# Kernel tuning notes

Measured on AMD Instinct MI355X. Metric: run time of the kernel, lower is better.

The kernel has to match this reference:

```python
import jax, jax.numpy as jnp
import numpy as np

PS = 4          # patch_size (square)
STRIDE = 2
PAD = (PS - 1) // 2
HEADS = 8
DIM = 256       # attn_dim == dim (kv_dim > dim, dim_reduc=1)
KV_DIM = 512
HD = DIM // HEADS
SCALE = HD ** -0.5
NP2 = PS * PS   # 16 elements per window


def _unfold(x, k, s, p):
    """torch.nn.functional.unfold: (B,C,H,W) -> (B, C*k*k, Ho*Wo)."""
    B, C, H, W = x.shape
    xp = jnp.pad(x, ((0, 0), (0, 0), (p, p), (p, p)))
    Ho = (H + 2 * p - k) // s + 1
    Wo = (W + 2 * p - k) // s + 1
    r = (jnp.arange(Ho) * s)[:, None] + jnp.arange(k)   # (Ho,k)
    c = (jnp.arange(Wo) * s)[:, None] + jnp.arange(k)   # (Wo,k)
    pt = xp[:, :, r][:, :, :, :, c]                     # (B,C,Ho,k,Wo,k)
    pt = pt.transpose(0, 1, 3, 5, 2, 4)                 # (B,C,k,k,Ho,Wo)
    return pt.reshape(B, C * k * k, Ho * Wo)


def _fold(y, C, Hout, Wout, k, s, p):
    """torch.nn.functional.fold: (B, C*k*k, Ho*Wo) -> (B,C,Hout,Wout), overlap-add."""
    B = y.shape[0]
    Ho = (Hout + 2 * p - k) // s + 1
    Wo = (Wout + 2 * p - k) // s + 1
    pt = y.reshape(B, C, k, k, Ho, Wo).transpose(0, 1, 4, 2, 5, 3)  # (B,C,Ho,k,Wo,k)
    r = (jnp.arange(Ho) * s)[:, None] + jnp.arange(k)
    c = (jnp.arange(Wo) * s)[:, None] + jnp.arange(k)
    out = jnp.zeros((B, C, Hout + 2 * p, Wout + 2 * p), y.dtype)
    out = out.at[:, :, r[:, :, None, None], c[None, None, :, :]].add(pt)
    return out[:, :, p:Hout + p, p:Wout + p]


def _patch_softmax(attn, Ht, Wt, Hb, Wb):
    """Normalize exp(attn) by per-bottom-pixel sums computed via a fold/unfold round trip
    (faithful to the original, including its reshape layout)."""
    a = jnp.exp(attn)                                                # (B*HtWt, H, 16, 1)
    s = a.reshape(-1, Ht * Wt, HEADS, NP2).transpose(0, 2, 3, 1)     # (B, H, 16, HtWt)
    s = s.reshape(-1, NP2, Ht * Wt)                                  # (B*H, 16, HtWt)
    s = _fold(s, 1, Hb, Wb, PS, STRIDE, PAD)                         # (B*H, 1, Hb, Wb)
    s = _unfold(s, PS, STRIDE, PAD).transpose(0, 2, 1)               # (B*H, HtWt, 16)
    s = jnp.where(s == 0, jnp.ones((), s.dtype), s)
    return a / s.reshape(-1, HEADS, NP2, 1)


def _forward(Xt, Xb, q_w, kv_w, proj_w, proj_b, rel_init, rel_bias, Ht, Wt, Hb, Wb):
    B, _, C = Xb.shape
    # im2col: gather 4x4 windows of the fine map, one window per coarse token
    Xbp = Xb.transpose(0, 2, 1).reshape(B, C, Hb, Wb)
    Xbp = _unfold(Xbp, PS, STRIDE, PAD)                              # (B, C*16, Ht*Wt)
    Xbp = Xbp.reshape(B, C, NP2, Ht * Wt).transpose(0, 3, 2, 1)
    Xbp = Xbp.reshape(B * Ht * Wt, NP2, C)                           # queries (top_down)
    Xtq = Xt.reshape(-1, 1, Xt.shape[-1])                            # (B*HtWt, 1, kv_dim)

    q = (Xbp @ q_w.T).reshape(-1, NP2, HEADS, HD).transpose(0, 2, 1, 3)  # (BHW,H,16,hd)
    kv = (Xtq @ kv_w.T).reshape(-1, 1, 2, HEADS, HD).transpose(2, 0, 3, 1, 4)
    k, v = kv[0], kv[1]                                              # (BHW,H,1,hd)

    attn = (q @ jnp.swapaxes(k, -2, -1)) * SCALE                     # (BHW,H,16,1)
    attn = attn + rel_init[:, None] + rel_bias[:, None]
    attn = _patch_softmax(attn, Ht, Wt, Hb, Wb)

    out = (attn @ v).transpose(0, 2, 1, 3).reshape(-1, NP2, DIM)     # (BHW,16,DIM)
    out = out.reshape(B, Ht * Wt, NP2, DIM).transpose(0, 3, 2, 1)
    out = out.reshape(B, DIM * NP2, Ht * Wt)
    out = _fold(out, DIM, Hb, Wb, PS, STRIDE, PAD)                   # (B,DIM,Hb,Wb)
    out = out.transpose(0, 2, 3, 1).reshape(B, Hb * Wb, DIM)
    return out @ proj_w.T + proj_b


def setup_inputs() -> dict:
    key = jax.random.key(0)
    ks = jax.random.split(key, 7)
    B, Ht, Wt, Hb, Wb = 4, 64, 64, 128, 128
    return {
        "Xt": jax.random.normal(ks[0], (B, Ht * Wt, KV_DIM), jnp.float32),
        "Xb": jax.random.normal(ks[1], (B, Hb * Wb, DIM), jnp.float32),
        "q_w": jax.random.normal(ks[2], (DIM, DIM), jnp.float32) * 0.02,
        "kv_w": jax.random.normal(ks[3], (2 * DIM, KV_DIM), jnp.float32) * 0.02,
        "proj_w": jax.random.normal(ks[4], (DIM, DIM), jnp.float32) * 0.02,
        "proj_b": jnp.zeros((DIM,), jnp.float32),
        "rel_init": jax.random.normal(ks[5], (NP2,), jnp.float32) * 0.02,
        "rel_bias": jax.random.normal(ks[6], (NP2,), jnp.float32) * 0.02,
        "Ht": Ht, "Wt": Wt, "Hb": Hb, "Wb": Wb,
    }


def reference(Xt, Xb, q_w, kv_w, proj_w, proj_b, rel_init, rel_bias, Ht, Wt, Hb, Wb):
    return _forward(Xt, Xb, q_w, kv_w, proj_w, proj_b, rel_init, rel_bias, Ht, Wt, Hb, Wb)
```

## Files before the change

kernel.cpp:

```cpp
#include <hip/hip_runtime.h>
#include <math.h>

constexpr int B_    = 4;
constexpr int HT    = 64,  WT = 64;
constexpr int HB    = 128, WB = 128;
constexpr int DIM   = 256;
constexpr int KVD   = 512;
constexpr int HEADS = 8;
constexpr int NP2   = 16;
constexpr int NPIX  = HB * WB;
constexpr int NWIN  = HT * WT;
constexpr float SCALE = 0.17677669529663687f;

using bf16x8 = __attribute__((ext_vector_type(8))) short;
using f32x4  = __attribute__((ext_vector_type(4))) float;

__device__ __forceinline__ unsigned short f2bf(float f) {
  union { float f; unsigned u; } v; v.f = f;
  unsigned r = v.u + 0x7fffu + ((v.u >> 16) & 1u);
  return (unsigned short)(r >> 16);
}

constexpr int NXT4  = B_ * NWIN * KVD / 4;
constexpr int NQW4  = DIM * DIM / 4;
constexpr int NKVW4 = KVD * KVD / 4;
constexpr int NCAST4 = NXT4 + NQW4 + NKVW4 + NQW4;

__global__ __launch_bounds__(256) void cast_all(
    const float* __restrict__ Xt, const float* __restrict__ qw,
    const float* __restrict__ kvw, const float* __restrict__ pw,
    unsigned short* __restrict__ Xth, unsigned short* __restrict__ qwh,
    unsigned short* __restrict__ kvwh, unsigned short* __restrict__ pwh)
{
  const int i = blockIdx.x * 256 + threadIdx.x;
  const float* src; unsigned short* dst; int off;
  if (i < NXT4)                     { src = Xt;  dst = Xth;  off = i; }
  else if (i < NXT4 + NQW4)         { src = qw;  dst = qwh;  off = i - NXT4; }
  else if (i < NXT4 + NQW4 + NKVW4) { src = kvw; dst = kvwh; off = i - NXT4 - NQW4; }
  else                              { src = pw;  dst = pwh;  off = i - NXT4 - NQW4 - NKVW4; }
  float4 v = ((const float4*)src)[off];
  ushort4 o;
  o.x = f2bf(v.x); o.y = f2bf(v.y); o.z = f2bf(v.z); o.w = f2bf(v.w);
  ((ushort4*)dst)[off] = o;
}

__global__ __launch_bounds__(256) void gemm_af32(
    const float* __restrict__ A, const unsigned short* __restrict__ Bw,
    unsigned short* __restrict__ C, int M, int N, int K)
{
  __shared__ unsigned short Ash[128 * 32];
  __shared__ unsigned short Bsh[128 * 32];

  const int tid  = threadIdx.x;
  const int wave = tid >> 6;
  const int lane = tid & 63;
  const int m0 = blockIdx.x * 128;
  const int n0 = blockIdx.y * 128;
  const int wm = (wave >> 1) * 64;
  const int wn = (wave & 1) * 64;

  const int c0 = wave * 64 + lane;
  const int c1 = 256 + c0;
  const int r0 = c0 >> 2, k0off = (c0 & 3) * 8;
  const int r1 = c1 >> 2, k1off = (c1 & 3) * 8;
  const int ldsOff0 = wave * 1024;
  const int ldsOff1 = 4096 + wave * 1024;

  f32x4 acc[4][4];
#pragma unroll
  for (int i = 0; i < 4; ++i)
#pragma unroll
    for (int j = 0; j < 4; ++j) { f32x4 z = {0.f, 0.f, 0.f, 0.f}; acc[i][j] = z; }

  const int fr = lane & 15;
  const int fk = (lane >> 4) * 8;

  for (int kk = 0; kk < K; kk += 32) {
    __syncthreads();
#pragma unroll
    for (int u = 0; u < 4; ++u) {
      const int c   = tid + u * 256;
      const int row = c >> 3;
      const int kq  = (c & 7) * 4;
      float4 v = *(const float4*)(A + (size_t)(m0 + row) * K + kk + kq);
      uint2 pk;
      pk.x = (unsigned)f2bf(v.x) | ((unsigned)f2bf(v.y) << 16);
      pk.y = (unsigned)f2bf(v.z) | ((unsigned)f2bf(v.w) << 16);
      *(uint2*)&Ash[row * 32 + kq] = pk;
    }
    const unsigned short* b0 = Bw + (size_t)(n0 + r0) * K + kk + k0off;
    const unsigned short* b1 = Bw + (size_t)(n0 + r1) * K + kk + k1off;
    __builtin_amdgcn_global_load_lds(
        (const __attribute__((address_space(1))) unsigned int*)b0,
        (__attribute__((address_space(3))) unsigned int*)((char*)Bsh + ldsOff0),
        16, 0, 0);
    __builtin_amdgcn_global_load_lds(
        (const __attribute__((address_space(1))) unsigned int*)b1,
        (__attribute__((address_space(3))) unsigned int*)((char*)Bsh + ldsOff1),
        16, 0, 0);
    __syncthreads();

    bf16x8 af[4], bfr[4];
#pragma unroll
    for (int t = 0; t < 4; ++t) {
      af[t]  = *(const bf16x8*)&Ash[(wm + t * 16 + fr) * 32 + fk];
      bfr[t] = *(const bf16x8*)&Bsh[(wn + t * 16 + fr) * 32 + fk];
    }
#pragma unroll
    for (int mt = 0; mt < 4; ++mt)
#pragma unroll
      for (int nt = 0; nt < 4; ++nt)
        acc[mt][nt] = __builtin_amdgcn_mfma_f32_16x16x32_bf16(
            af[mt], bfr[nt], acc[mt][nt], 0, 0, 0);
  }

  const int col0 = lane & 15;
  const int rb   = (lane >> 4) * 4;
#pragma unroll
  for (int mt = 0; mt < 4; ++mt)
#pragma unroll
    for (int nt = 0; nt < 4; ++nt) {
      const int col = n0 + wn + nt * 16 + col0;
#pragma unroll
      for (int r = 0; r < 4; ++r) {
        const int row = m0 + wm + mt * 16 + rb + r;
        C[(size_t)row * N + col] = f2bf(acc[mt][nt][r]);
      }
    }
}

template<bool BF16_OUT, bool BIAS>
__global__ __launch_bounds__(256) void gemm_bf16(
    const unsigned short* __restrict__ A, const unsigned short* __restrict__ Bw,
    const float* __restrict__ bias, void* __restrict__ C,
    int M, int N, int K)
{
  __shared__ unsigned short Ash[128 * 32];
  __shared__ unsigned short Bsh[128 * 32];

  const int tid  = threadIdx.x;
  const int wave = tid >> 6;
  const int lane = tid & 63;
  const int m0 = blockIdx.x * 128;
  const int n0 = blockIdx.y * 128;
  const int wm = (wave >> 1) * 64;
  const int wn = (wave & 1) * 64;

  const int c0 = wave * 64 + lane;
  const int c1 = 256 + c0;
  const int r0 = c0 >> 2, k0off = (c0 & 3) * 8;
  const int r1 = c1 >> 2, k1off = (c1 & 3) * 8;
  const int ldsOff0 = wave * 1024;
  const int ldsOff1 = 4096 + wave * 1024;

  f32x4 acc[4][4];
#pragma unroll
  for (int i = 0; i < 4; ++i)
#pragma unroll
    for (int j = 0; j < 4; ++j) { f32x4 z = {0.f, 0.f, 0.f, 0.f}; acc[i][j] = z; }

  const int fr = lane & 15;
  const int fk = (lane >> 4) * 8;

  for (int kk = 0; kk < K; kk += 32) {
    __syncthreads();
    const unsigned short* a0 = A  + (size_t)(m0 + r0) * K + kk + k0off;
    const unsigned short* a1 = A  + (size_t)(m0 + r1) * K + kk + k1off;
    const unsigned short* b0 = Bw + (size_t)(n0 + r0) * K + kk + k0off;
    const unsigned short* b1 = Bw + (size_t)(n0 + r1) * K + kk + k1off;
    __builtin_amdgcn_global_load_lds(
        (const __attribute__((address_space(1))) unsigned int*)a0,
        (__attribute__((address_space(3))) unsigned int*)((char*)Ash + ldsOff0),
        16, 0, 0);
    __builtin_amdgcn_global_load_lds(
        (const __attribute__((address_space(1))) unsigned int*)a1,
        (__attribute__((address_space(3))) unsigned int*)((char*)Ash + ldsOff1),
        16, 0, 0);
    __builtin_amdgcn_global_load_lds(
        (const __attribute__((address_space(1))) unsigned int*)b0,
        (__attribute__((address_space(3))) unsigned int*)((char*)Bsh + ldsOff0),
        16, 0, 0);
    __builtin_amdgcn_global_load_lds(
        (const __attribute__((address_space(1))) unsigned int*)b1,
        (__attribute__((address_space(3))) unsigned int*)((char*)Bsh + ldsOff1),
        16, 0, 0);
    __syncthreads();

    bf16x8 af[4], bfr[4];
#pragma unroll
    for (int t = 0; t < 4; ++t) {
      af[t]  = *(const bf16x8*)&Ash[(wm + t * 16 + fr) * 32 + fk];
      bfr[t] = *(const bf16x8*)&Bsh[(wn + t * 16 + fr) * 32 + fk];
    }
#pragma unroll
    for (int mt = 0; mt < 4; ++mt)
#pragma unroll
      for (int nt = 0; nt < 4; ++nt)
        acc[mt][nt] = __builtin_amdgcn_mfma_f32_16x16x32_bf16(
            af[mt], bfr[nt], acc[mt][nt], 0, 0, 0);
  }

  const int col0 = lane & 15;
  const int rb   = (lane >> 4) * 4;
#pragma unroll
  for (int mt = 0; mt < 4; ++mt)
#pragma unroll
    for (int nt = 0; nt < 4; ++nt) {
      const int col = n0 + wn + nt * 16 + col0;
      float bv = BIAS ? bias[col] : 0.f;
#pragma unroll
      for (int r = 0; r < 4; ++r) {
        const int row = m0 + wm + mt * 16 + rb + r;
        const float v = acc[mt][nt][r] + bv;
        if (BF16_OUT) ((unsigned short*)C)[(size_t)row * N + col] = f2bf(v);
        else          ((float*)C)[(size_t)row * N + col] = v;
      }
    }
}

__global__ __launch_bounds__(256) void es_kernel(
    const unsigned short* __restrict__ Qh, const unsigned short* __restrict__ KVh,
    const float* __restrict__ rel_init, const float* __restrict__ rel_bias,
    float* __restrict__ E, float* __restrict__ S)
{
  const int idx = blockIdx.x * 256 + threadIdx.x;
  const int h = idx & 7;
  const int x = (idx >> 3) & 127;
  const int y = (idx >> 10) & 127;
  const int b = idx >> 17;

  const uint4* qp = (const uint4*)(Qh + ((size_t)((b << 14) + y * WB + x)) * DIM + h * 32);
  uint4 q0 = qp[0], q1 = qp[1], q2 = qp[2], q3 = qp[3];
  const unsigned qa[16] = {q0.x,q0.y,q0.z,q0.w, q1.x,q1.y,q1.z,q1.w,
                           q2.x,q2.y,q2.z,q2.w, q3.x,q3.y,q3.z,q3.w};

  const int ilo = max(0, (y - 1) >> 1), ihi = min(HT - 1, (y + 1) >> 1);
  const int jlo = max(0, (x - 1) >> 1), jhi = min(WT - 1, (x + 1) >> 1);

  float s = 0.f;
  for (int i = ilo; i <= ihi; ++i)
    for (int j = jlo; j <= jhi; ++j) {
      const int w = i * WT + j;
      const int p = (y + 1 - 2 * i) * 4 + (x + 1 - 2 * j);
      const uint4* kp = (const uint4*)(KVh + ((size_t)((b << 12) + w)) * KVD + h * 32);
      uint4 k0 = kp[0], k1 = kp[1], k2 = kp[2], k3 = kp[3];
      const unsigned ka[16] = {k0.x,k0.y,k0.z,k0.w, k1.x,k1.y,k1.z,k1.w,
                               k2.x,k2.y,k2.z,k2.w, k3.x,k3.y,k3.z,k3.w};
      float acc = 0.f;
#pragma unroll
      for (int q = 0; q < 16; ++q) {
        acc = fmaf(__uint_as_float(qa[q] << 16),
                   __uint_as_float(ka[q] << 16), acc);
        acc = fmaf(__uint_as_float(qa[q] & 0xffff0000u),
                   __uint_as_float(ka[q] & 0xffff0000u), acc);
      }
      const float e = expf(acc * SCALE + rel_init[p] + rel_bias[p]);
      E[((size_t)((b << 12) + w)) * 128 + h * NP2 + p] = e;
      s += e;
    }
  S[(size_t)((b * HEADS + h) << 14) + y * WB + x] = s;
}

__global__ __launch_bounds__(256) void r_kernel(
    const float* __restrict__ E, const float* __restrict__ S,
    float* __restrict__ R)
{
  const int idx = blockIdx.x * 256 + threadIdx.x;
  const int b  = idx >> 19;
  const int r  = idx & 524287;
  const int w  = r >> 7;
  const int t7 = r & 127;
  const int h  = t7 >> 4, p = t7 & 15;

  const int h_eff = w >> 9;
  const int w_eff = ((w & 511) << 3) + h;
  const int i2 = w_eff >> 6, j2 = w_eff & 63;
  const int y2 = 2 * i2 + (p >> 2) - 1;
  const int x2 = 2 * j2 + (p & 3) - 1;
  float s = 1.f;
  if ((unsigned)y2 < (unsigned)HB && (unsigned)x2 < (unsigned)WB)
    s = S[(size_t)((b * HEADS + h_eff) * NPIX) + y2 * WB + x2];
  R[idx] = E[idx] / s;
}

__global__ __launch_bounds__(256) void o_kernel(
    const float* __restrict__ R, const unsigned short* __restrict__ KVh,
    unsigned short* __restrict__ out_pre)
{
  const int t  = threadIdx.x;
  const int pg = blockIdx.x * 8 + (t >> 5);
  const int b  = pg >> 14;
  const int yx = pg & 16383;
  const int y  = yx >> 7, x = yx & 127;
  const int c8 = t & 31;
  const int h  = c8 >> 2;

  const int ilo = max(0, (y - 1) >> 1), ihi = min(HT - 1, (y + 1) >> 1);
  const int jlo = max(0, (x - 1) >> 1), jhi = min(WT - 1, (x + 1) >> 1);

  float acc[8] = {};
  for (int i = ilo; i <= ihi; ++i)
    for (int j = jlo; j <= jhi; ++j) {
      const int w = i * WT + j;
      const int p = (y + 1 - 2 * i) * 4 + (x + 1 - 2 * j);
      const float rr = R[((size_t)(b * NWIN + w)) * 128 + h * NP2 + p];
      const uint4 v = *(const uint4*)(KVh + ((size_t)(b * NWIN + w)) * KVD + 256 + c8 * 8);
      const unsigned vv[4] = {v.x, v.y, v.z, v.w};
#pragma unroll
      for (int q = 0; q < 4; ++q) {
        acc[2*q]   = fmaf(rr, __uint_as_float(vv[q] << 16),         acc[2*q]);
        acc[2*q+1] = fmaf(rr, __uint_as_float(vv[q] & 0xffff0000u), acc[2*q+1]);
      }
    }

  uint4 ov;
  ov.x = (unsigned)f2bf(acc[0]) | ((unsigned)f2bf(acc[1]) << 16);
  ov.y = (unsigned)f2bf(acc[2]) | ((unsigned)f2bf(acc[3]) << 16);
  ov.z = (unsigned)f2bf(acc[4]) | ((unsigned)f2bf(acc[5]) << 16);
  ov.w = (unsigned)f2bf(acc[6]) | ((unsigned)f2bf(acc[7]) << 16);
  *(uint4*)(out_pre + (size_t)pg * DIM + c8 * 8) = ov;
}

extern "C" void kernel_launch(void* const* d_in, const int* in_sizes, int n_in,
                              void* d_out, int out_size, void* d_ws, size_t ws_size,
                              hipStream_t stream) {
  const float* Xt       = (const float*)d_in[0];
  const float* Xb       = (const float*)d_in[1];
  const float* q_w      = (const float*)d_in[2];
  const float* kv_w     = (const float*)d_in[3];
  const float* proj_w   = (const float*)d_in[4];
  const float* proj_b   = (const float*)d_in[5];
  const float* rel_init = (const float*)d_in[6];
  const float* rel_bias = (const float*)d_in[7];
  float* out = (float*)d_out;

  char* ws = (char*)d_ws;
  const size_t nXb = (size_t)B_ * NPIX * DIM;
  const size_t nXt = (size_t)B_ * NWIN * KVD;
  const size_t nQW = (size_t)DIM * DIM;
  const size_t nKVW = (size_t)KVD * KVD;
  unsigned short* Qh   = (unsigned short*)ws;  ws += nXb * 2;
  unsigned short* Xth  = (unsigned short*)ws;  ws += nXt * 2;
  unsigned short* KVh  = (unsigned short*)ws;  ws += nXt * 2;
  float*          E    = (float*)ws;           ws += (size_t)B_ * NWIN * 128 * 4;
  float*          S    = (float*)ws;           ws += (size_t)B_ * HEADS * NPIX * 4;
  unsigned short* qwh  = (unsigned short*)ws;  ws += nQW * 2;
  unsigned short* kvwh = (unsigned short*)ws;  ws += nKVW * 2;
  unsigned short* pwh  = (unsigned short*)ws;  ws += nQW * 2;
  float*          R    = (float*)Xth;
  unsigned short* Oh   = Qh;

  const dim3 blk(256);

  cast_all<<<dim3(NCAST4 / 256), blk, 0, stream>>>(
      Xt, q_w, kv_w, proj_w, Xth, qwh, kvwh, pwh);

  gemm_af32<<<dim3(B_ * NPIX / 128, DIM / 128), blk, 0, stream>>>(
      Xb, qwh, Qh, B_ * NPIX, DIM, DIM);

  gemm_bf16<true, false><<<dim3(B_ * NWIN / 128, KVD / 128), blk, 0, stream>>>(
      Xth, kvwh, nullptr, KVh, B_ * NWIN, KVD, KVD);

  es_kernel<<<dim3(B_ * NPIX * HEADS / 256), blk, 0, stream>>>(
      Qh, KVh, rel_init, rel_bias, E, S);

  r_kernel<<<dim3(B_ * NWIN * 128 / 256), blk, 0, stream>>>(E, S, R);

  o_kernel<<<dim3(B_ * NPIX / 8), blk, 0, stream>>>(R, KVh, Oh);

  gemm_bf16<false, true><<<dim3(B_ * NPIX / 128, DIM / 128), blk, 0, stream>>>(
      Oh, pwh, proj_b, out, B_ * NPIX, DIM, DIM);
}
```

Measured before the change: 262.0 us.

## Merge Q and KV projection GEMMs into one launch with wider N tiles

Combines the Q projection (fp32 A, converted in-kernel) and the KV projection into a single kernel that interleaves blocks of the two GEMMs, and widens the N tile to 256 for the 256-wide outputs so the A tile is read once per row block. It also register-prefetches the next fp32 A tile before the MFMA work to overlap global loads, and uses a cheaper perm-based bf16 pack. The intent is to cut launch count, redundant A reads and load latency. The cost is more registers per thread with launch_bounds(256,2), and a bf16 rounding mode that differs from the round-to-nearest-even f2bf.

```diff
diff --git a/kernel.cpp b/kernel.cpp
--- a/kernel.cpp
+++ b/kernel.cpp
@@ -20,6 +20,11 @@
   unsigned r = v.u + 0x7fffu + ((v.u >> 16) & 1u);
   return (unsigned short)(r >> 16);
 }
+__device__ __forceinline__ unsigned pack_bf16(float x, float y) {
+  unsigned ux = __float_as_uint(x) + 0x8000u;
+  unsigned uy = __float_as_uint(y) + 0x8000u;
+  return __builtin_amdgcn_perm(uy, ux, 0x07060302u);
+}
 
 constexpr int NXT4  = B_ * NWIN * KVD / 4;
 constexpr int NQW4  = DIM * DIM / 4;
@@ -44,74 +49,93 @@
   ((ushort4*)dst)[off] = o;
 }
 
-__global__ __launch_bounds__(256) void gemm_af32(
-    const float* __restrict__ A, const unsigned short* __restrict__ Bw,
-    unsigned short* __restrict__ C, int M, int N, int K)
-{
-  __shared__ unsigned short Ash[128 * 32];
-  __shared__ unsigned short Bsh[128 * 32];
-
+template<bool AF32, int BN, bool BF16_OUT, bool BIAS>
+__device__ __forceinline__ void gemm_core(
+    const void* __restrict__ Ap, const unsigned short* __restrict__ Bw,
+    const float* __restrict__ bias, void* __restrict__ Cp,
+    int M, int N, int K, int bx, int by,
+    unsigned short* Ash, unsigned short* Bsh)
+{
+  constexpr int NT = BN / 32;
   const int tid  = threadIdx.x;
   const int wave = tid >> 6;
   const int lane = tid & 63;
-  const int m0 = blockIdx.x * 128;
-  const int n0 = blockIdx.y * 128;
+  const int m0 = bx * 128;
+  const int n0 = by * BN;
   const int wm = (wave >> 1) * 64;
-  const int wn = (wave & 1) * 64;
-
-  const int c0 = wave * 64 + lane;
-  const int c1 = 256 + c0;
-  const int r0 = c0 >> 2, k0off = (c0 & 3) * 8;
-  const int r1 = c1 >> 2, k1off = (c1 & 3) * 8;
-  const int ldsOff0 = wave * 1024;
-  const int ldsOff1 = 4096 + wave * 1024;
-
-  f32x4 acc[4][4];
+  const int wn = (wave & 1) * (BN / 2);
+
+  f32x4 acc[4][NT];
 #pragma unroll
   for (int i = 0; i < 4; ++i)
 #pragma unroll
-    for (int j = 0; j < 4; ++j) { f32x4 z = {0.f, 0.f, 0.f, 0.f}; acc[i][j] = z; }
+    for (int j = 0; j < NT; ++j) { f32x4 z = {0.f, 0.f, 0.f, 0.f}; acc[i][j] = z; }
+
+  const float* Af = (const float*)Ap;
+  float4 areg[4];
+  auto loadA = [&](int kk) {
+#pragma unroll
+    for (int u = 0; u < 4; ++u) {
+      const int c = u * 256 + tid, row = c >> 3, kq = (c & 7) * 4;
+      areg[u] = *(const float4*)(Af + (size_t)(m0 + row) * K + kk + kq);
+    }
+  };
+  if constexpr (AF32) loadA(0);
 
   const int fr = lane & 15;
   const int fk = (lane >> 4) * 8;
 
   for (int kk = 0; kk < K; kk += 32) {
     __syncthreads();
-#pragma unroll
-    for (int u = 0; u < 4; ++u) {
-      const int c   = tid + u * 256;
-      const int row = c >> 3;
-      const int kq  = (c & 7) * 4;
-      float4 v = *(const float4*)(A + (size_t)(m0 + row) * K + kk + kq);
-      uint2 pk;
-      pk.x = (unsigned)f2bf(v.x) | ((unsigned)f2bf(v.y) << 16);
-      pk.y = (unsigned)f2bf(v.z) | ((unsigned)f2bf(v.w) << 16);
-      *(uint2*)&Ash[row * 32 + kq] = pk;
-    }
-    const unsigned short* b0 = Bw + (size_t)(n0 + r0) * K + kk + k0off;
-    const unsigned short* b1 = Bw + (size_t)(n0 + r1) * K + kk + k1off;
-    __builtin_amdgcn_global_load_lds(
-        (const __attribute__((address_space(1))) unsigned int*)b0,
-        (__attribute__((address_space(3))) unsigned int*)((char*)Bsh + ldsOff0),
-        16, 0, 0);
-    __builtin_amdgcn_global_load_lds(
-        (const __attribute__((address_space(1))) unsigned int*)b1,
-        (__attribute__((address_space(3))) unsigned int*)((char*)Bsh + ldsOff1),
-        16, 0, 0);
+    if constexpr (AF32) {
+#pragma unroll
+      for (int u = 0; u < 4; ++u) {
+        const int c = u * 256 + tid, row = c >> 3, kq = (c & 7) * 4;
+        uint2 pk;
+        pk.x = pack_bf16(areg[u].x, areg[u].y);
+        pk.y = pack_bf16(areg[u].z, areg[u].w);
+        *(uint2*)&Ash[row * 32 + kq] = pk;
+      }
+    } else {
+      const unsigned short* Ab = (const unsigned short*)Ap;
+#pragma unroll
+      for (int i = 0; i < 2; ++i) {
+        const int c = i * 256 + wave * 64 + lane, row = c >> 2, ko = (c & 3) * 8;
+        __builtin_amdgcn_global_load_lds(
+            (const __attribute__((address_space(1))) unsigned int*)
+                (Ab + (size_t)(m0 + row) * K + kk + ko),
+            (__attribute__((address_space(3))) unsigned int*)
+                ((char*)Ash + i * 4096 + wave * 1024),
+            16, 0, 0);
+      }
+    }
+#pragma unroll
+    for (int i = 0; i < BN / 64; ++i) {
+      const int c = i * 256 + wave * 64 + lane, row = c >> 2, ko = (c & 3) * 8;
+      __builtin_amdgcn_global_load_lds(
+          (const __attribute__((address_space(1))) unsigned int*)
+              (Bw + (size_t)(n0 + row) * K + kk + ko),
+          (__attribute__((address_space(3))) unsigned int*)
+              ((char*)Bsh + i * 4096 + wave * 1024),
+          16, 0, 0);
+    }
     __syncthreads();
 
-    bf16x8 af[4], bfr[4];
-#pragma unroll
-    for (int t = 0; t < 4; ++t) {
-      af[t]  = *(const bf16x8*)&Ash[(wm + t * 16 + fr) * 32 + fk];
-      bfr[t] = *(const bf16x8*)&Bsh[(wn + t * 16 + fr) * 32 + fk];
-    }
+    if constexpr (AF32) { if (kk + 32 < K) loadA(kk + 32); }
+
+    bf16x8 af[4], bf[NT];
+#pragma unroll
+    for (int t = 0; t < 4; ++t)
+      af[t] = *(const bf16x8*)&Ash[(wm + t * 16 + fr) * 32 + fk];
+#pragma unroll
+    for (int t = 0; t < NT; ++t)
+      bf[t] = *(const bf16x8*)&Bsh[(wn + t * 16 + fr) * 32 + fk];
 #pragma unroll
     for (int mt = 0; mt < 4; ++mt)
 #pragma unroll
-      for (int nt = 0; nt < 4; ++nt)
+      for (int nt = 0; nt < NT; ++nt)
         acc[mt][nt] = __builtin_amdgcn_mfma_f32_16x16x32_bf16(
-            af[mt], bfr[nt], acc[mt][nt], 0, 0, 0);
+            af[mt], bf[nt], acc[mt][nt], 0, 0, 0);
   }
 
   const int col0 = lane & 15;
@@ -119,103 +143,46 @@
 #pragma unroll
   for (int mt = 0; mt < 4; ++mt)
 #pragma unroll
-    for (int nt = 0; nt < 4; ++nt) {
-      const int col = n0 + wn + nt * 16 + col0;
-#pragma unroll
-      for (int r = 0; r < 4; ++r) {
-        const int row = m0 + wm + mt * 16 + rb + r;
-        C[(size_t)row * N + col] = f2bf(acc[mt][nt][r]);
-      }
-    }
-}
-
-template<bool BF16_OUT, bool BIAS>
-__global__ __launch_bounds__(256) void gemm_bf16(
-    const unsigned short* __restrict__ A, const unsigned short* __restrict__ Bw,
-    const float* __restrict__ bias, void* __restrict__ C,
-    int M, int N, int K)
-{
-  __shared__ unsigned short Ash[128 * 32];
-  __shared__ unsigned short Bsh[128 * 32];
-
-  const int tid  = threadIdx.x;
-  const int wave = tid >> 6;
-  const int lane = tid & 63;
-  const int m0 = blockIdx.x * 128;
-  const int n0 = blockIdx.y * 128;
-  const int wm = (wave >> 1) * 64;
-  const int wn = (wave & 1) * 64;
-
-  const int c0 = wave * 64 + lane;
-  const int c1 = 256 + c0;
-  const int r0 = c0 >> 2, k0off = (c0 & 3) * 8;
-  const int r1 = c1 >> 2, k1off = (c1 & 3) * 8;
-  const int ldsOff0 = wave * 1024;
-  const int ldsOff1 = 4096 + wave * 1024;
-
-  f32x4 acc[4][4];
-#pragma unroll
-  for (int i = 0; i < 4; ++i)
-#pragma unroll
-    for (int j = 0; j < 4; ++j) { f32x4 z = {0.f, 0.f, 0.f, 0.f}; acc[i][j] = z; }
-
-  const int fr = lane & 15;
-  const int fk = (lane >> 4) * 8;
-
-  for (int kk = 0; kk < K; kk += 32) {
-    __syncthreads();
-    const unsigned short* a0 = A  + (size_t)(m0 + r0) * K + kk + k0off;
-    const unsigned short* a1 = A  + (size_t)(m0 + r1) * K + kk + k1off;
-    const unsigned short* b0 = Bw + (size_t)(n0 + r0) * K + kk + k0off;
-    const unsigned short* b1 = Bw + (size_t)(n0 + r1) * K + kk + k1off;
-    __builtin_amdgcn_global_load_lds(
-        (const __attribute__((address_space(1))) unsigned int*)a0,
-        (__attribute__((address_space(3))) unsigned int*)((char*)Ash + ldsOff0),
-        16, 0, 0);
-    __builtin_amdgcn_global_load_lds(
-        (const __attribute__((address_space(1))) unsigned int*)a1,
-        (__attribute__((address_space(3))) unsigned int*)((char*)Ash + ldsOff1),
-        16, 0, 0);
-    __builtin_amdgcn_global_load_lds(
-        (const __attribute__((address_space(1))) unsigned int*)b0,
-        (__attribute__((address_space(3))) unsigned int*)((char*)Bsh + ldsOff0),
-        16, 0, 0);
-    __builtin_amdgcn_global_load_lds(
-        (const __attribute__((address_space(1))) unsigned int*)b1,
-        (__attribute__((address_space(3))) unsigned int*)((char*)Bsh + ldsOff1),
-        16, 0, 0);
-    __syncthreads();
-
-    bf16x8 af[4], bfr[4];
-#pragma unroll
-    for (int t = 0; t < 4; ++t) {
-      af[t]  = *(const bf16x8*)&Ash[(wm + t * 16 + fr) * 32 + fk];
-      bfr[t] = *(const bf16x8*)&Bsh[(wn + t * 16 + fr) * 32 + fk];
-    }
-#pragma unroll
-    for (int mt = 0; mt < 4; ++mt)
-#pragma unroll
-      for (int nt = 0; nt < 4; ++nt)
-        acc[mt][nt] = __builtin_amdgcn_mfma_f32_16x16x32_bf16(
-            af[mt], bfr[nt], acc[mt][nt], 0, 0, 0);
-  }
-
-  const int col0 = lane & 15;
-  const int rb   = (lane >> 4) * 4;
-#pragma unroll
-  for (int mt = 0; mt < 4; ++mt)
-#pragma unroll
-    for (int nt = 0; nt < 4; ++nt) {
+    for (int nt = 0; nt < NT; ++nt) {
       const int col = n0 + wn + nt * 16 + col0;
       float bv = BIAS ? bias[col] : 0.f;
 #pragma unroll
       for (int r = 0; r < 4; ++r) {
         const int row = m0 + wm + mt * 16 + rb + r;
         const float v = acc[mt][nt][r] + bv;
-        if (BF16_OUT) ((unsigned short*)C)[(size_t)row * N + col] = f2bf(v);
-        else          ((float*)C)[(size_t)row * N + col] = v;
-      }
-    }
+        if (BF16_OUT) ((unsigned short*)Cp)[(size_t)row * N + col] = f2bf(v);
+        else          ((float*)Cp)[(size_t)row * N + col] = v;
+      }
+    }
+}
+
+__global__ __launch_bounds__(256, 2) void g12_kernel(
+    const float* __restrict__ Xb, const unsigned short* __restrict__ qwh,
+    unsigned short* __restrict__ Qh,
+    const unsigned short* __restrict__ Xth, const unsigned short* __restrict__ kvwh,
+    unsigned short* __restrict__ KVh)
+{
+  __shared__ unsigned short Ash[128 * 32];
+  __shared__ unsigned short Bsh[256 * 32];
+  const int id = blockIdx.x;
+  if ((id & 1) == 0) {
+    gemm_core<true, 256, true, false>(Xb, qwh, nullptr, Qh,
+        B_ * NPIX, DIM, DIM, id >> 1, 0, Ash, Bsh);
+  } else {
+    const int t = id >> 1;
+    gemm_core<false, 128, true, false>(Xth, kvwh, nullptr, KVh,
+        B_ * NWIN, KVD, KVD, t >> 2, t & 3, Ash, Bsh);
+  }
+}
+
+__global__ __launch_bounds__(256, 2) void g3_kernel(
+    const unsigned short* __restrict__ Oh, const unsigned short* __restrict__ pwh,
+    const float* __restrict__ pb, float* __restrict__ out)
+{
+  __shared__ unsigned short Ash[128 * 32];
+  __shared__ unsigned short Bsh[256 * 32];
+  gemm_core<false, 256, false, true>(Oh, pwh, pb, out,
+      B_ * NPIX, DIM, DIM, blockIdx.x, 0, Ash, Bsh);
 }
 
 __global__ __launch_bounds__(256) void es_kernel(
@@ -355,11 +322,7 @@
   cast_all<<<dim3(NCAST4 / 256), blk, 0, stream>>>(
       Xt, q_w, kv_w, proj_w, Xth, qwh, kvwh, pwh);
 
-  gemm_af32<<<dim3(B_ * NPIX / 128, DIM / 128), blk, 0, stream>>>(
-      Xb, qwh, Qh, B_ * NPIX, DIM, DIM);
-
-  gemm_bf16<true, false><<<dim3(B_ * NWIN / 128, KVD / 128), blk, 0, stream>>>(
-      Xth, kvwh, nullptr, KVh, B_ * NWIN, KVD, KVD);
+  g12_kernel<<<dim3(1024), blk, 0, stream>>>(Xb, qwh, Qh, Xth, kvwh, KVh);
 
   es_kernel<<<dim3(B_ * NPIX * HEADS / 256), blk, 0, stream>>>(
       Qh, KVh, rel_init, rel_bias, E, S);
@@ -368,6 +331,5 @@
 
   o_kernel<<<dim3(B_ * NPIX / 8), blk, 0, stream>>>(R, KVh, Oh);
 
-  gemm_bf16<false, true><<<dim3(B_ * NPIX / 128, DIM / 128), blk, 0, stream>>>(
-      Oh, pwh, proj_b, out, B_ * NPIX, DIM, DIM);
-}
+  g3_kernel<<<dim3(B_ * NPIX / 128), blk, 0, stream>>>(Oh, pwh, proj_b, out);
+}
```

Result: faster. 253.3 us (-3.3%).
